# Kernel optimization log

Measured on AMD Instinct MI355X. Metric: run time of the kernel, lower is better.

## Reference

```python
import jax, jax.numpy as jnp
import numpy as np

OT_GAMMA = 1.0
OT_EPS = 1e-06
OT_ITER = 20
L2_EPS = 1e-12  # F.normalize default eps


def _forward(ft, fs):
    # X = cat(ft, fs): [2n, d]
    X = jnp.concatenate([ft, fs], axis=0)
    # cosine similarity (F.normalize p=2 along dim=1, then X Xn^T)
    Xn = X / jnp.maximum(jnp.linalg.norm(X, axis=1, keepdims=True), L2_EPS)
    C = Xn @ Xn.T  # [2n, 2n]
    n = C.shape[0] // 2
    M = C[:n, n:]  # teacher-student cross block [n, n]
    # zscore_normalize (torch.std is unbiased -> ddof=1)
    M = (M - M.mean()) / jnp.std(M, ddof=1)

    # sinkhorn(1 - M[None], gamma, eps, maxiters), logspace=False, r=c=None
    Mb = (1.0 - M)[None, :, :]  # [1, n, n]
    B, H, W = Mb.shape
    r = 1.0 / H
    c = 1.0 / W
    P0 = jnp.exp(-OT_GAMMA * (Mb - jnp.min(Mb, axis=2, keepdims=True)))

    def step(carry, _):
        P, done = carry
        alpha = P.sum(axis=2, keepdims=True)        # [B, H, 1]
        P1 = P / alpha * r                          # row-normalize
        beta = P1.sum(axis=1, keepdims=True)        # [B, 1, W]
        new_done = done | (jnp.max(jnp.abs(beta - c)) <= OT_EPS)
        # torch breaks AFTER row-normalization when converged
        P2 = jnp.where(new_done, P1, P1 / beta * c)
        P_next = jnp.where(done, P, P2)             # freeze once converged
        return (P_next, new_done), None

    (P, _), _ = jax.lax.scan(step, (P0, jnp.array(False)), None, length=OT_ITER)
    P = P[0]  # squeeze batch -> [n, n]

    # doubly_normalize
    P = P / P.sum(axis=1, keepdims=True)
    P = P / P.sum(axis=0, keepdims=True)

    # torch.norm(A, 2) with no dim flattens -> Frobenius norm
    I = jnp.eye(P.shape[1], dtype=P.dtype)
    loss_ot = jnp.linalg.norm(P - I)
    return loss_ot, P, M


def setup_inputs() -> dict:
    key = jax.random.key(0)
    k1, k2 = jax.random.split(key)
    ft = jax.random.normal(k1, (4096, 1024), dtype=jnp.float32)
    fs = jax.random.normal(k2, (4096, 1024), dtype=jnp.float32)
    return {"ft": ft, "fs": fs}


def reference(ft, fs):
    return _forward(ft, fs)
```

## Files before the change

kernel.cpp:

```cpp
#include <hip/hip_runtime.h>
#include <stdint.h>
#include <math.h>


#define NN 4096
#define DIM 1024
#define OT_ITERS 20
#define OT_EPS_F 1e-6f
#define RC (1.0f/4096.0f)
#define RPB 16
#define SBT 512

typedef __bf16 bf16_t;
typedef _Float16 half_t;
typedef __bf16 bf16x8 __attribute__((ext_vector_type(8)));
typedef _Float16 halfx8 __attribute__((ext_vector_type(8)));
typedef float floatx4 __attribute__((ext_vector_type(4)));

typedef __attribute__((address_space(1))) void gv_t;
typedef __attribute__((address_space(3))) void lv_t;

__device__ __forceinline__ void gld_lds16(const void* g, void* lds_uniform) {
  uint32_t loff = (uint32_t)(uintptr_t)lds_uniform;
  loff = (uint32_t)__builtin_amdgcn_readfirstlane((int)loff);
  __builtin_amdgcn_global_load_lds((gv_t*)(uintptr_t)g, (lv_t*)(uintptr_t)loff, 16, 0, 0);
}

__device__ __forceinline__ void gbar(uint32_t* bar, uint32_t g) {
  __syncthreads();
  if (threadIdx.x == 0) {
    uint32_t* cnt = bar + ((blockIdx.x >> 5) * 64);
    uint32_t* root = bar + 512;
    uint32_t* gen = bar + 576;
    if (__hip_atomic_fetch_add(cnt, 1u, __ATOMIC_RELEASE, __HIP_MEMORY_SCOPE_AGENT) == 31u) {
      __hip_atomic_store(cnt, 0u, __ATOMIC_RELAXED, __HIP_MEMORY_SCOPE_AGENT);
      if (__hip_atomic_fetch_add(root, 1u, __ATOMIC_ACQ_REL, __HIP_MEMORY_SCOPE_AGENT) == 7u) {
        __hip_atomic_store(root, 0u, __ATOMIC_RELAXED, __HIP_MEMORY_SCOPE_AGENT);
        __hip_atomic_store(gen, g, __ATOMIC_RELEASE, __HIP_MEMORY_SCOPE_AGENT);
      }
    }
    while (__hip_atomic_load(gen, __ATOMIC_RELAXED, __HIP_MEMORY_SCOPE_AGENT) < g)
      __builtin_amdgcn_s_sleep(1);
    __builtin_amdgcn_fence(__ATOMIC_ACQUIRE, "agent");
  }
  __syncthreads();
}

__global__ void init_ws(float* scal, uint32_t* bar) {
  int i = blockIdx.x * 256 + threadIdx.x;
  if (i < 8) ((uint32_t*)scal)[i] = 0u;
  if (i < 640) bar[i] = 0u;
}

__global__ __launch_bounds__(256) void norm_rows(const float* __restrict__ X,
                                                 bf16_t* __restrict__ Y) {
  int tid = threadIdx.x;
  int wave = tid >> 6, lane = tid & 63;
  int row = blockIdx.x * 4 + wave;
  const float* xr = X + (size_t)row * DIM;
  float xv[16];
  float ss = 0.f;
#pragma unroll
  for (int k = 0; k < 16; k++) { xv[k] = xr[lane + 64 * k]; ss += xv[k] * xv[k]; }
#pragma unroll
  for (int off = 1; off < 64; off <<= 1) ss += __shfl_xor(ss, off, 64);
  float inv = rsqrtf(ss);
  bf16_t* yr = Y + (size_t)row * DIM;
#pragma unroll
  for (int k = 0; k < 16; k++) yr[lane + 64 * k] = (bf16_t)(xv[k] * inv);
}

__global__ __launch_bounds__(256) void gemm_bt(const bf16_t* __restrict__ A,
                                               const bf16_t* __restrict__ B,
                                               float* __restrict__ C,
                                               float* __restrict__ sumArr,
                                               float* __restrict__ sqArr,
                                               float* __restrict__ rmPart) {
  __shared__ __align__(16) bf16_t As[128 * 32];
  __shared__ __align__(16) bf16_t Bs[128 * 32];
  __shared__ float sred[8];
  int tid = threadIdx.x;
  int wave = tid >> 6, lane = tid & 63;
  int quad = lane >> 4, l16 = lane & 15;
  int bm = blockIdx.y, bn = blockIdx.x;
  int waveM = wave >> 1, waveN = wave & 1;
  floatx4 acc[4][4] = {};

  for (int k0 = 0; k0 < DIM; k0 += 32) {
#pragma unroll
    for (int t = 0; t < 2; t++) {
      int cbase = t * 256 + wave * 64;
      int c = cbase + lane;
      int row = c >> 2, kc = c & 3;
      gld_lds16(A + (size_t)(bm * 128 + row) * DIM + (k0 + kc * 8), (char*)As + (size_t)cbase * 16);
      gld_lds16(B + (size_t)(bn * 128 + row) * DIM + (k0 + kc * 8), (char*)Bs + (size_t)cbase * 16);
    }
    __syncthreads();
    bf16x8 af[4], bfr[4];
#pragma unroll
    for (int mt = 0; mt < 4; mt++)
      af[mt] = *(const bf16x8*)(As + (waveM * 64 + mt * 16 + l16) * 32 + quad * 8);
#pragma unroll
    for (int nt = 0; nt < 4; nt++)
      bfr[nt] = *(const bf16x8*)(Bs + (waveN * 64 + nt * 16 + l16) * 32 + quad * 8);
#pragma unroll
    for (int mt = 0; mt < 4; mt++)
#pragma unroll
      for (int nt = 0; nt < 4; nt++)
        acc[mt][nt] = __builtin_amdgcn_mfma_f32_16x16x32_bf16(af[mt], bfr[nt], acc[mt][nt], 0, 0, 0);
    __syncthreads();
  }

  float lsum = 0.f, lsq = 0.f;
#pragma unroll
  for (int mt = 0; mt < 4; mt++) {
#pragma unroll
    for (int r = 0; r < 4; r++) {
      int gi = bm * 128 + waveM * 64 + mt * 16 + quad * 4 + r;
      float rmax = -3.4e38f;
#pragma unroll
      for (int nt = 0; nt < 4; nt++) {
        float vv = acc[mt][nt][r];
        int gj = bn * 128 + waveN * 64 + nt * 16 + l16;
        C[(size_t)gi * NN + gj] = vv;
        lsum += vv;
        lsq += vv * vv;
        rmax = fmaxf(rmax, vv);
      }
#pragma unroll
      for (int off = 1; off < 16; off <<= 1) rmax = fmaxf(rmax, __shfl_xor(rmax, off, 64));
      if (l16 == 0) rmPart[(size_t)(bn * 2 + waveN) * NN + gi] = rmax;
    }
  }
#pragma unroll
  for (int off = 1; off < 64; off <<= 1) {
    lsum += __shfl_xor(lsum, off, 64);
    lsq += __shfl_xor(lsq, off, 64);
  }
  if (lane == 0) { sred[wave] = lsum; sred[4 + wave] = lsq; }
  __syncthreads();
  if (tid == 0) {
    int bid = bm * 32 + bn;
    sumArr[bid] = sred[0] + sred[1] + sred[2] + sred[3];
    sqArr[bid] = sred[4] + sred[5] + sred[6] + sred[7];
  }
}

__global__ __launch_bounds__(SBT, 1) void sinkhorn_full(
    float* __restrict__ M,
    float* __restrict__ P,
    float* __restrict__ scal,
    const float* __restrict__ sumArr,
    const float* __restrict__ sqArr,
    const float* __restrict__ rmPart,
    float* __restrict__ t,
    float* __restrict__ s,
    float* __restrict__ tg,
    float* __restrict__ devArr,
    uint32_t* __restrict__ bar,
    float* __restrict__ out) {
  __shared__ float red[8 * RPB];
  __shared__ float u_lds[RPB];
  __shared__ float scratch[SBT];
  __shared__ float rowmax_l[RPB];
  __shared__ double dred[16];
  __shared__ float stat_l[2];

  const int b = blockIdx.x;
  const int tid = threadIdx.x;
  const int wave = tid >> 6, lane = tid & 63;
  const int g0 = b * RPB;
  const int c0 = tid * 8;
  uint32_t bg = 0;

  {
    double ds = (double)sumArr[tid] + (double)sumArr[tid + 512];
    double dq = (double)sqArr[tid] + (double)sqArr[tid + 512];
#pragma unroll
    for (int off = 1; off < 64; off <<= 1) {
      ds += __shfl_xor(ds, off, 64);
      dq += __shfl_xor(dq, off, 64);
    }
    if (lane == 0) { dred[wave] = ds; dred[8 + wave] = dq; }
  }
  {
    int row = tid >> 5, half = tid & 31;
    float rm = fmaxf(rmPart[(size_t)(half * 2) * NN + g0 + row],
                     rmPart[(size_t)(half * 2 + 1) * NN + g0 + row]);
#pragma unroll
    for (int off = 1; off < 32; off <<= 1) rm = fmaxf(rm, __shfl_xor(rm, off, 64));
    if (half == 0) rowmax_l[row] = rm;
  }
  __syncthreads();
  if (tid == 0) {
    double sum = 0.0, sumsq = 0.0;
#pragma unroll
    for (int w = 0; w < 8; w++) { sum += dred[w]; sumsq += dred[8 + w]; }
    double Nd = (double)NN * (double)NN;
    double meand = sum / Nd;
    double var = (sumsq - sum * sum / Nd) / (Nd - 1.0);
    stat_l[0] = (float)meand;
    stat_l[1] = (float)(1.0 / sqrt(var));
  }
  __syncthreads();
  const float mean = stat_l[0], istd = stat_l[1];

  halfx8 kreg[RPB];
#pragma unroll
  for (int i = 0; i < RPB; i++) {
    float rmax = rowmax_l[i];
    float* mrow = M + (size_t)(g0 + i) * NN + c0;
    float4 a = *(const float4*)mrow;
    float4 bb = *(const float4*)(mrow + 4);
    float4 sa, sb;
    sa.x = (a.x - mean) * istd;  sa.y = (a.y - mean) * istd;
    sa.z = (a.z - mean) * istd;  sa.w = (a.w - mean) * istd;
    sb.x = (bb.x - mean) * istd; sb.y = (bb.y - mean) * istd;
    sb.z = (bb.z - mean) * istd; sb.w = (bb.w - mean) * istd;
    *(float4*)mrow = sa;
    *(float4*)(mrow + 4) = sb;
    halfx8 kp;
    kp[0] = (half_t)__expf((a.x - rmax) * istd);
    kp[1] = (half_t)__expf((a.y - rmax) * istd);
    kp[2] = (half_t)__expf((a.z - rmax) * istd);
    kp[3] = (half_t)__expf((a.w - rmax) * istd);
    kp[4] = (half_t)__expf((bb.x - rmax) * istd);
    kp[5] = (half_t)__expf((bb.y - rmax) * istd);
    kp[6] = (half_t)__expf((bb.z - rmax) * istd);
    kp[7] = (half_t)__expf((bb.w - rmax) * istd);
    kreg[i] = kp;
  }

  float vr[8];
#pragma unroll
  for (int q = 0; q < 8; q++) vr[q] = 1.0f;

  auto matvec_phase = [&](float scale) {
    float part[RPB];
#pragma unroll
    for (int i = 0; i < RPB; i++) {
      float p = 0.f;
#pragma unroll
      for (int q = 0; q < 8; q++) p += (float)kreg[i][q] * vr[q];
      part[i] = p;
    }
#pragma unroll
    for (int off = 1; off < 64; off <<= 1)
#pragma unroll
      for (int i = 0; i < RPB; i++) part[i] += __shfl_xor(part[i], off, 64);
    if (lane == 0) {
#pragma unroll
      for (int i = 0; i < RPB; i++) red[wave * RPB + i] = part[i];
    }
    __syncthreads();
    if (tid < RPB) {
      float dsum = 0.f;
#pragma unroll
      for (int w = 0; w < 8; w++) dsum += red[w * RPB + tid];
      u_lds[tid] = scale / dsum;
    }
    __syncthreads();
    float ta[8];
#pragma unroll
    for (int q = 0; q < 8; q++) ta[q] = 0.f;
#pragma unroll
    for (int i = 0; i < RPB; i++) {
      float ui = u_lds[i];
#pragma unroll
      for (int q = 0; q < 8; q++) ta[q] += (float)kreg[i][q] * ui;
    }
    float* tgb = tg + (size_t)b * NN;
#pragma unroll
    for (int q = 0; q < 8; q++) tgb[c0 + q] = ta[q];
  };

  auto colreduce = [&]() -> float {
    int jl = tid & 15, seg = tid >> 4;
    int j = g0 + jl;
    float acc = 0.f;
#pragma unroll
    for (int m = 0; m < 8; m++) acc += tg[(size_t)(seg * 8 + m) * NN + j];
    scratch[tid] = acc;
    __syncthreads();
    float tn = 0.f;
    if (tid < RPB) {
#pragma unroll
      for (int k = 0; k < 32; k++) tn += scratch[tid + RPB * k];
    }
    return tn;
  };

  bool frozen = false;
  for (int it = 0; it < OT_ITERS; it++) {
    if (it > 0) {
      float4 t0 = *(const float4*)(t + c0);
      float4 t1 = *(const float4*)(t + c0 + 4);
      vr[0] = RC / t0.x; vr[1] = RC / t0.y; vr[2] = RC / t0.z; vr[3] = RC / t0.w;
      vr[4] = RC / t1.x; vr[5] = RC / t1.y; vr[6] = RC / t1.z; vr[7] = RC / t1.w;
    }
    matvec_phase(RC);
    gbar(bar, ++bg);
    float tn = colreduce();
    if (tid < RPB) {
      int j = g0 + tid;
      float vj = (it == 0) ? 1.0f : (RC / t[j]);
      float dev = fabsf(vj * tn - RC);
      t[j] = tn;
#pragma unroll
      for (int off = 1; off < RPB; off <<= 1) dev = fmaxf(dev, __shfl_xor(dev, off, 64));
      if (tid == 0) devArr[b] = dev;
    }
    gbar(bar, ++bg);
    float x = (tid < 256) ? devArr[tid] : 0.f;
#pragma unroll
    for (int off = 1; off < 64; off <<= 1) x = fmaxf(x, __shfl_xor(x, off, 64));
    if (lane == 0 && wave < 4) scratch[300 + wave] = x;
    __syncthreads();
    float md = fmaxf(fmaxf(scratch[300], scratch[301]), fmaxf(scratch[302], scratch[303]));
    if (md <= OT_EPS_F) { frozen = true; break; }
  }
  if (!frozen) {
#pragma unroll
    for (int q = 0; q < 8; q++) vr[q] = RC / t[c0 + q];
  }

  matvec_phase(1.0f);
  gbar(bar, ++bg);
  float tn = colreduce();
  if (tid < RPB) s[g0 + tid] = tn;
  gbar(bar, ++bg);

  float4 s0 = *(const float4*)(s + c0);
  float4 s1 = *(const float4*)(s + c0 + 4);
  float isv[8] = {1.0f / s0.x, 1.0f / s0.y, 1.0f / s0.z, 1.0f / s0.w,
                  1.0f / s1.x, 1.0f / s1.y, 1.0f / s1.z, 1.0f / s1.w};
  float ls = 0.f;
#pragma unroll
  for (int i = 0; i < RPB; i++) {
    int gi = g0 + i;
    float wi = u_lds[i];
    float* prow = P + (size_t)gi * NN;
#pragma unroll
    for (int q = 0; q < 8; q++) {
      float p = (float)kreg[i][q] * wi * isv[q];
      prow[c0 + q] = p;
      float d = p - ((gi == c0 + q) ? 1.0f : 0.0f);
      ls += d * d;
    }
  }
#pragma unroll
  for (int off = 1; off < 64; off <<= 1) ls += __shfl_xor(ls, off, 64);
  __syncthreads();
  if (lane == 0) red[wave] = ls;
  __syncthreads();
  if (tid == 0) {
    float tot = 0.f;
#pragma unroll
    for (int w = 0; w < 8; w++) tot += red[w];
    atomicAdd(&scal[4], tot);
  }
  gbar(bar, ++bg);
  if (b == 0 && tid == 0) out[0] = sqrtf(scal[4]);
}

extern "C" void kernel_launch(void* const* d_in, const int* in_sizes, int n_in, void* d_out,
                              int out_size, void* d_ws, size_t ws_size, hipStream_t stream) {
  const float* ft = (const float*)d_in[0];
  const float* fs = (const float*)d_in[1];
  float* out = (float*)d_out;

  char* ws = (char*)d_ws;
  bf16_t* A = (bf16_t*)ws;
  bf16_t* B = (bf16_t*)(ws + (8u << 20));
  float* tg = (float*)(ws + (16u << 20));
  float* fbase = (float*)(ws + (24u << 20));
  float* t = fbase;
  float* s = fbase + 4096;
  float* devArr = fbase + 8192;
  float* scal = fbase + 8448;
  uint32_t* bar = (uint32_t*)(fbase + 8704);
  float* sumArr = fbase + 10240;
  float* sqArr = fbase + 11264;
  float* rmPart = fbase + 16384;

  float* P_out = out + 1;
  float* M_out = out + 1 + (size_t)NN * NN;

  init_ws<<<3, 256, 0, stream>>>(scal, bar);
  norm_rows<<<1024, 256, 0, stream>>>(ft, A);
  norm_rows<<<1024, 256, 0, stream>>>(fs, B);
  gemm_bt<<<dim3(32, 32), 256, 0, stream>>>(A, B, M_out, sumArr, sqArr, rmPart);

  sinkhorn_full<<<256, SBT, 0, stream>>>(M_out, P_out, scal, sumArr, sqArr, rmPart, t, s, tg,
                                         devArr, bar, out);
}
```

Measured before the change: 373.0 us.

## Replace hierarchical atomic grid barrier with per-block flags and merge init/normalize launches

Swaps the two-level counter grid barrier for a flag array: each block publishes its generation number, and one wave per block polls all 256 flags with vector loads and a wave-wide all-reduce. This takes the serialized atomic fetch-add chain off each barrier's critical path. It also folds workspace init and both row-normalization launches into one kernel, saving two launches. In exchange, every block now polls all 256 flags, which adds memory traffic while waiting.

```diff
diff --git a/kernel.cpp b/kernel.cpp
--- a/kernel.cpp
+++ b/kernel.cpp
@@ -26,37 +26,40 @@
   __builtin_amdgcn_global_load_lds((gv_t*)(uintptr_t)g, (lv_t*)(uintptr_t)loff, 16, 0, 0);
 }
 
-__device__ __forceinline__ void gbar(uint32_t* bar, uint32_t g) {
-  __syncthreads();
-  if (threadIdx.x == 0) {
-    uint32_t* cnt = bar + ((blockIdx.x >> 5) * 64);
-    uint32_t* root = bar + 512;
-    uint32_t* gen = bar + 576;
-    if (__hip_atomic_fetch_add(cnt, 1u, __ATOMIC_RELEASE, __HIP_MEMORY_SCOPE_AGENT) == 31u) {
-      __hip_atomic_store(cnt, 0u, __ATOMIC_RELAXED, __HIP_MEMORY_SCOPE_AGENT);
-      if (__hip_atomic_fetch_add(root, 1u, __ATOMIC_ACQ_REL, __HIP_MEMORY_SCOPE_AGENT) == 7u) {
-        __hip_atomic_store(root, 0u, __ATOMIC_RELAXED, __HIP_MEMORY_SCOPE_AGENT);
-        __hip_atomic_store(gen, g, __ATOMIC_RELEASE, __HIP_MEMORY_SCOPE_AGENT);
-      }
-    }
-    while (__hip_atomic_load(gen, __ATOMIC_RELAXED, __HIP_MEMORY_SCOPE_AGENT) < g)
+__device__ __forceinline__ void gbar(uint32_t* flags, uint32_t g) {
+  __syncthreads();
+  int tid = threadIdx.x;
+  if (tid == 0)
+    __hip_atomic_store(&flags[blockIdx.x], g, __ATOMIC_RELEASE, __HIP_MEMORY_SCOPE_AGENT);
+  if (tid < 64) {
+    const uint32_t* f = flags + (tid << 2);
+    for (;;) {
+      uint32_t a = __hip_atomic_load(f + 0, __ATOMIC_RELAXED, __HIP_MEMORY_SCOPE_AGENT);
+      uint32_t b = __hip_atomic_load(f + 1, __ATOMIC_RELAXED, __HIP_MEMORY_SCOPE_AGENT);
+      uint32_t c = __hip_atomic_load(f + 2, __ATOMIC_RELAXED, __HIP_MEMORY_SCOPE_AGENT);
+      uint32_t d = __hip_atomic_load(f + 3, __ATOMIC_RELAXED, __HIP_MEMORY_SCOPE_AGENT);
+      uint32_t mn = min(min(a, b), min(c, d));
+      if (__all(mn >= g)) break;
       __builtin_amdgcn_s_sleep(1);
+    }
     __builtin_amdgcn_fence(__ATOMIC_ACQUIRE, "agent");
   }
   __syncthreads();
 }
 
-__global__ void init_ws(float* scal, uint32_t* bar) {
-  int i = blockIdx.x * 256 + threadIdx.x;
-  if (i < 8) ((uint32_t*)scal)[i] = 0u;
-  if (i < 640) bar[i] = 0u;
-}
-
-__global__ __launch_bounds__(256) void norm_rows(const float* __restrict__ X,
-                                                 bf16_t* __restrict__ Y) {
+__global__ __launch_bounds__(256) void norm_rows2(const float* __restrict__ ft,
+                                                  const float* __restrict__ fs,
+                                                  bf16_t* __restrict__ A,
+                                                  bf16_t* __restrict__ B,
+                                                  float* __restrict__ scal,
+                                                  uint32_t* __restrict__ flags) {
+  int gb = blockIdx.x;
+  const float* X = (gb < 1024) ? ft : fs;
+  bf16_t* Y = (gb < 1024) ? A : B;
+  int bb = gb & 1023;
   int tid = threadIdx.x;
   int wave = tid >> 6, lane = tid & 63;
-  int row = blockIdx.x * 4 + wave;
+  int row = bb * 4 + wave;
   const float* xr = X + (size_t)row * DIM;
   float xv[16];
   float ss = 0.f;
@@ -68,6 +71,10 @@
   bf16_t* yr = Y + (size_t)row * DIM;
 #pragma unroll
   for (int k = 0; k < 16; k++) yr[lane + 64 * k] = (bf16_t)(xv[k] * inv);
+  if (gb == 0) {
+    flags[tid] = 0u;
+    if (tid < 8) ((uint32_t*)scal)[tid] = 0u;
+  }
 }
 
 __global__ __launch_bounds__(256) void gemm_bt(const bf16_t* __restrict__ A,
@@ -157,7 +164,7 @@
     float* __restrict__ s,
     float* __restrict__ tg,
     float* __restrict__ devArr,
-    uint32_t* __restrict__ bar,
+    uint32_t* __restrict__ flags,
     float* __restrict__ out) {
   __shared__ float red[8 * RPB];
   __shared__ float u_lds[RPB];
@@ -299,7 +306,7 @@
       vr[4] = RC / t1.x; vr[5] = RC / t1.y; vr[6] = RC / t1.z; vr[7] = RC / t1.w;
     }
     matvec_phase(RC);
-    gbar(bar, ++bg);
+    gbar(flags, ++bg);
     float tn = colreduce();
     if (tid < RPB) {
       int j = g0 + tid;
@@ -310,7 +317,7 @@
       for (int off = 1; off < RPB; off <<= 1) dev = fmaxf(dev, __shfl_xor(dev, off, 64));
       if (tid == 0) devArr[b] = dev;
     }
-    gbar(bar, ++bg);
+    gbar(flags, ++bg);
     float x = (tid < 256) ? devArr[tid] : 0.f;
 #pragma unroll
     for (int off = 1; off < 64; off <<= 1) x = fmaxf(x, __shfl_xor(x, off, 64));
@@ -325,10 +332,10 @@
   }
 
   matvec_phase(1.0f);
-  gbar(bar, ++bg);
+  gbar(flags, ++bg);
   float tn = colreduce();
   if (tid < RPB) s[g0 + tid] = tn;
-  gbar(bar, ++bg);
+  gbar(flags, ++bg);
 
   float4 s0 = *(const float4*)(s + c0);
   float4 s1 = *(const float4*)(s + c0 + 4);
@@ -359,7 +366,7 @@
     for (int w = 0; w < 8; w++) tot += red[w];
     atomicAdd(&scal[4], tot);
   }
-  gbar(bar, ++bg);
+  gbar(flags, ++bg);
   if (b == 0 && tid == 0) out[0] = sqrtf(scal[4]);
 }
 
@@ -378,7 +385,7 @@
   float* s = fbase + 4096;
   float* devArr = fbase + 8192;
   float* scal = fbase + 8448;
-  uint32_t* bar = (uint32_t*)(fbase + 8704);
+  uint32_t* flags = (uint32_t*)(fbase + 8704);
   float* sumArr = fbase + 10240;
   float* sqArr = fbase + 11264;
   float* rmPart = fbase + 16384;
@@ -386,11 +393,9 @@
   float* P_out = out + 1;
   float* M_out = out + 1 + (size_t)NN * NN;
 
-  init_ws<<<3, 256, 0, stream>>>(scal, bar);
-  norm_rows<<<1024, 256, 0, stream>>>(ft, A);
-  norm_rows<<<1024, 256, 0, stream>>>(fs, B);
+  norm_rows2<<<2048, 256, 0, stream>>>(ft, fs, A, B, scal, flags);
   gemm_bt<<<dim3(32, 32), 256, 0, stream>>>(A, B, M_out, sumArr, sqArr, rmPart);
 
   sinkhorn_full<<<256, SBT, 0, stream>>>(M_out, P_out, scal, sumArr, sqArr, rmPart, t, s, tg,
-                                         devArr, bar, out);
-}
+                                         devArr, flags, out);
+}
```

Result: slower. 382.4 us (+2.5%).
